# Kernel tuning notes

Hardware: AMD Instinct MI355X
Metric: run time of the kernel (lower is better)

Reference implementation:

```python
import jax, jax.numpy as jnp
import numpy as np

RES = 14
N = RES * RES
NH = 8
KD = 32
D = 128   # attn_ratio * key_dim
DH = 1024 # D * NH
DIM = 384
B = 128
SCALE = KD ** -0.5


def _bias_idxs():
    pts = [(i, j) for i in range(RES) for j in range(RES)]
    offs, idxs = {}, []
    for p1 in pts:
        for p2 in pts:
            o = (abs(p1[0] - p2[0]), abs(p1[1] - p2[1]))
            offs.setdefault(o, len(offs))
            idxs.append(offs[o])
    return np.array(idxs, np.int32).reshape(N, N), len(offs)

BIAS_IDXS, NUM_OFF = _bias_idxs()  # (N, N), 196 distinct |offset| pairs


def setup_inputs() -> dict:
    key = jax.random.key(0)
    ks = jax.random.split(key, 32)
    g = lambda i, shape, s=0.05: jax.random.normal(ks[i], shape, jnp.float32) * s
    pos = lambda i, shape: jax.random.uniform(ks[i], shape, jnp.float32, minval=0.5, maxval=1.5)
    return dict(
        x=jax.random.normal(ks[0], (B, DIM, RES, RES), jnp.float32),
        qw=g(1, (NH * KD, DIM)), qb=g(2, (NH * KD,)), q_s=pos(3, (NH * KD,)), q_t=g(4, (NH * KD,)),
        kw=g(5, (NH * KD, DIM)), kb=g(6, (NH * KD,)), k_s=pos(7, (NH * KD,)), k_t=g(8, (NH * KD,)),
        vw=g(9, (DH, DIM)), vb=g(10, (DH,)), v_s=pos(11, (DH,)), v_t=g(12, (DH,)),
        lvw=g(13, (DH, 3, 3)), lvb=g(14, (DH,)), lv_s=pos(15, (DH,)), lv_t=g(16, (DH,)),
        th1w=g(17, (NH, NH), 0.3), th1b=g(18, (NH,)),
        th2w=g(19, (NH, NH), 0.3), th2b=g(20, (NH,)),
        ab=g(21, (NH, NUM_OFF)),
        pw=g(22, (DIM, DH)), pb=g(23, (DIM,)), p_s=pos(24, (DIM,)), p_t=g(25, (DIM,)),
    )


def _c(v):
    return v[None, :, None, None]


def conv1x1_bn(x, w, b, s, t):
    # 1x1 conv (NCHW) + eval-mode BN folded to per-channel affine
    y = jnp.einsum('bchw,oc->bohw', x, w) + _c(b)
    return y * _c(s) + _c(t)


def reference(x, qw, qb, q_s, q_t, kw, kb, k_s, k_t, vw, vb, v_s, v_t,
              lvw, lvb, lv_s, lv_t, th1w, th1b, th2w, th2b, ab,
              pw, pb, p_s, p_t):
    Bb = x.shape[0]
    # q,k: (B, NH, N, KD)
    q = conv1x1_bn(x, qw, qb, q_s, q_t).reshape(Bb, NH, KD, N).transpose(0, 1, 3, 2)
    k = conv1x1_bn(x, kw, kb, k_s, k_t).reshape(Bb, NH, KD, N).transpose(0, 1, 3, 2)
    v4 = conv1x1_bn(x, vw, vb, v_s, v_t)  # (B, DH, RES, RES)
    # local depthwise 3x3 conv + BN on v
    vl = jax.lax.conv_general_dilated(
        v4, lvw.reshape(DH, 1, 3, 3), window_strides=(1, 1), padding='SAME',
        dimension_numbers=('NCHW', 'OIHW', 'NCHW'), feature_group_count=DH)
    vl = (vl + _c(lvb)) * _c(lv_s) + _c(lv_t)
    v = v4.reshape(Bb, NH, D, N).transpose(0, 1, 3, 2)  # (B, NH, N, D)

    attn = jnp.einsum('bhid,bhjd->bhij', q, k) * SCALE
    attn = attn + ab[:, BIAS_IDXS][None]  # relative-position bias (1, NH, N, N)
    attn = jnp.einsum('bhij,gh->bgij', attn, th1w) + _c(th1b)  # talking head 1
    attn = jax.nn.softmax(attn, axis=-1)
    attn = jnp.einsum('bhij,gh->bgij', attn, th2w) + _c(th2b)  # talking head 2

    o = jnp.einsum('bhij,bhjd->bhid', attn, v)  # (B, NH, N, D)
    o = o.transpose(0, 1, 3, 2).reshape(Bb, DH, RES, RES) + vl
    o = jax.nn.relu(o)
    return conv1x1_bn(o, pw, pb, p_s, p_t)
```

## Files before the change

### kernel.cpp

```cpp
#include <hip/hip_runtime.h>
#include <hip/hip_bf16.h>
#include <stdint.h>

typedef __hip_bfloat16 bf16;
typedef short short4v __attribute__((ext_vector_type(4)));
typedef short short8 __attribute__((ext_vector_type(8)));
typedef float f32x4 __attribute__((ext_vector_type(4)));

#define NB 128
#define NPIX 196
#define NPAD 208
#define VP 224
#define QROWS 208
#define NH 8
#define KD 32
#define DHEAD 128
#define DH 1024
#define DIM 384
#define SCALE 0.17677669529663687f

__device__ __forceinline__ float b2f(bf16 v) { return __bfloat162float(v); }
__device__ __forceinline__ bf16 f2b(float f) { return __float2bfloat16(f); }
__device__ __forceinline__ float us2f(unsigned short u) {
  union { unsigned int i; float f; } v; v.i = (unsigned int)u << 16; return v.f;
}
__device__ __forceinline__ short f2us(float f) {
  bf16 b = __float2bfloat16(f);
  return *(short*)&b;
}

__device__ __forceinline__ void gll16(const void* g, void* l) {
  auto gp = reinterpret_cast<const uint32_t __attribute__((address_space(1)))*>(
      reinterpret_cast<uintptr_t>(g));
  auto lp = reinterpret_cast<uint32_t __attribute__((address_space(3)))*>(
      reinterpret_cast<uintptr_t>(l));
  __builtin_amdgcn_global_load_lds(gp, lp, 16, 0, 0);
}

__global__ __launch_bounds__(256) void k_cvt4(const float* __restrict__ s0,
                                              const float* __restrict__ s1,
                                              const float* __restrict__ s2,
                                              const float* __restrict__ s3,
                                              bf16* __restrict__ dst) {
  int i = blockIdx.x * 256 + threadIdx.x;
  if (i >= 983040) return;
  const float* src; int o;
  if (i < 98304)       { src = s0; o = i; }
  else if (i < 196608) { src = s1; o = i - 98304; }
  else if (i < 589824) { src = s2; o = i - 196608; }
  else                 { src = s3; o = i - 589824; }
  dst[i] = f2b(src[o]);
}

__global__ __launch_bounds__(256) void k_xt(const float* __restrict__ x,
                                            bf16* __restrict__ XT) {
  __shared__ bf16 tile[32][33];
  int ct = blockIdx.x, nt = blockIdx.y, b = blockIdx.z;
  int c0 = ct * 32, n0 = nt * 32;
  int tc = threadIdx.x >> 5, tn = threadIdx.x & 31;
#pragma unroll
  for (int r = 0; r < 4; ++r) {
    int c = tc + r * 8;
    int n = n0 + tn;
    float v = 0.f;
    if (n < NPIX) v = x[((size_t)b * DIM + c0 + c) * NPIX + n];
    tile[c][tn] = f2b(v);
  }
  __syncthreads();
#pragma unroll
  for (int r = 0; r < 4; ++r) {
    int n = n0 + tc + r * 8;
    if (n < NPAD) XT[((size_t)b * NPAD + n) * DIM + c0 + tn] = tile[tn][tc + r * 8];
  }
}

__global__ __launch_bounds__(256, 2) void k_qkv2(
    const bf16* __restrict__ Wf, const bf16* __restrict__ XT,
    const float* __restrict__ qb, const float* __restrict__ qs, const float* __restrict__ qt,
    const float* __restrict__ kb, const float* __restrict__ ks, const float* __restrict__ kt,
    const float* __restrict__ vb, const float* __restrict__ vs, const float* __restrict__ vt,
    bf16* __restrict__ qf, bf16* __restrict__ kf, bf16* __restrict__ v4) {
  __shared__ __align__(16) char lds[2][32768];
  const int NWG = 12 * 208;
  int id = blockIdx.x;
  int id2 = (id & 7) * (NWG >> 3) + (id >> 3);
  int mt = id2 % 12, nt = id2 / 12;
  int m0 = mt * 128, n0 = nt * 128;
  int tid = threadIdx.x, lane = tid & 63;
  int wv = tid >> 6, wm = wv >> 1, wn = wv & 1;

  f32x4 acc[4][4];
#pragma unroll
  for (int mi = 0; mi < 4; ++mi)
#pragma unroll
    for (int ni = 0; ni < 4; ++ni)
#pragma unroll
      for (int r = 0; r < 4; ++r) acc[mi][ni][r] = 0.f;

  auto stage = [&](int buf, int t) {
    int k0 = t * 64;
#pragma unroll
    for (int j = 0; j < 4; ++j) {
      int gi = tid + j * 256;
      int row = gi >> 3, g = gi & 7;
      int sk = k0 + ((g ^ (row & 7)) << 3);
      gll16(Wf + (size_t)(m0 + row) * DIM + sk, &lds[buf][gi * 16]);
      gll16(XT + (size_t)(n0 + row) * DIM + sk, &lds[buf][16384 + gi * 16]);
    }
  };
  auto compute = [&](int buf) {
    const char* Ab = lds[buf];
    const char* Bb = lds[buf] + 16384;
    int kq = lane >> 4, il = lane & 15;
#pragma unroll
    for (int ksb = 0; ksb < 2; ++ksb) {
      int G = ksb * 4 + kq;
      short8 af[4], bfr[4];
#pragma unroll
      for (int mi = 0; mi < 4; ++mi) {
        int row = wm * 64 + mi * 16 + il;
        af[mi] = *(const short8*)(Ab + row * 128 + ((G ^ (row & 7)) << 4));
      }
#pragma unroll
      for (int ni = 0; ni < 4; ++ni) {
        int row = wn * 64 + ni * 16 + il;
        bfr[ni] = *(const short8*)(Bb + row * 128 + ((G ^ (row & 7)) << 4));
      }
#pragma unroll
      for (int mi = 0; mi < 4; ++mi)
#pragma unroll
        for (int ni = 0; ni < 4; ++ni)
          acc[mi][ni] = __builtin_amdgcn_mfma_f32_16x16x32_bf16(af[mi], bfr[ni], acc[mi][ni], 0, 0, 0);
    }
  };

  stage(0, 0);
  __syncthreads();
  for (int t = 0; t < 6; ++t) {
    if (t < 5) stage((t + 1) & 1, t + 1);
    compute(t & 1);
    __syncthreads();
  }

  int cq = lane >> 4, cn = lane & 15;
#pragma unroll
  for (int mi = 0; mi < 4; ++mi) {
    int mbase = m0 + wm * 64 + mi * 16;
    const float *bp, *sp, *tp;
    int segbase, segid;
    if (mbase < 256)      { bp = qb; sp = qs; tp = qt; segbase = 0;   segid = 0; }
    else if (mbase < 512) { bp = kb; sp = ks; tp = kt; segbase = 256; segid = 1; }
    else                  { bp = vb; sp = vs; tp = vt; segbase = 512; segid = 2; }
#pragma unroll
    for (int r = 0; r < 4; ++r) {
      int ms = mbase - segbase + cq * 4 + r;
      float bi = bp[ms], sc = sp[ms], tt = tp[ms];
#pragma unroll
      for (int ni = 0; ni < 4; ++ni) {
        int n = n0 + wn * 64 + ni * 16 + cn;
        int b = n / NPAD;
        int nn = n - b * NPAD;
        float y = (acc[mi][ni][r] + bi) * sc + tt;
        y = (nn < NPIX) ? y : 0.f;
        if (segid == 2) {
          v4[((size_t)b * DH + ms) * VP + nn] = f2b(y);
        } else {
          bf16* dst = segid ? kf : qf;
          dst[(((size_t)b * NH + (ms >> 5)) * QROWS + nn) * KD + (ms & 31)] = f2b(y);
        }
      }
    }
  }
}

__global__ __launch_bounds__(256) void k_vpad(bf16* __restrict__ v4) {
  int i = blockIdx.x * 256 + threadIdx.x;
  int tot = NB * DH * 16;
  if (i < tot) {
    int row = i >> 4, c = i & 15;
    v4[(size_t)row * VP + 208 + c] = f2b(0.f);
  }
}

__global__ __launch_bounds__(256, 2) void k_p2(
    const bf16* __restrict__ Pw, const bf16* __restrict__ OT,
    const float* __restrict__ pb, const float* __restrict__ ps, const float* __restrict__ pt,
    float* __restrict__ out) {
  __shared__ __align__(16) char lds[2][32768];
  const int NWG = 3 * 208;
  int id = blockIdx.x;
  int id2 = (id & 7) * (NWG >> 3) + (id >> 3);
  int mt = id2 % 3, nt = id2 / 3;
  int m0 = mt * 128, n0 = nt * 128;
  int tid = threadIdx.x, lane = tid & 63;
  int wv = tid >> 6, wm = wv >> 1, wn = wv & 1;

  f32x4 acc[4][4];
#pragma unroll
  for (int mi = 0; mi < 4; ++mi)
#pragma unroll
    for (int ni = 0; ni < 4; ++ni)
#pragma unroll
      for (int r = 0; r < 4; ++r) acc[mi][ni][r] = 0.f;

  auto stage = [&](int buf, int t) {
    int k0 = t * 64;
#pragma unroll
    for (int j = 0; j < 4; ++j) {
      int gi = tid + j * 256;
      int row = gi >> 3, g = gi & 7;
      int sk = k0 + ((g ^ (row & 7)) << 3);
      gll16(Pw + (size_t)(m0 + row) * DH + sk, &lds[buf][gi * 16]);
      gll16(OT + (size_t)(n0 + row) * DH + sk, &lds[buf][16384 + gi * 16]);
    }
  };
  auto compute = [&](int buf) {
    const char* Ab = lds[buf];
    const char* Bb = lds[buf] + 16384;
    int kq = lane >> 4, il = lane & 15;
#pragma unroll
    for (int ksb = 0; ksb < 2; ++ksb) {
      int G = ksb * 4 + kq;
      short8 af[4], bfr[4];
#pragma unroll
      for (int mi = 0; mi < 4; ++mi) {
        int row = wm * 64 + mi * 16 + il;
        af[mi] = *(const short8*)(Ab + row * 128 + ((G ^ (row & 7)) << 4));
      }
#pragma unroll
      for (int ni = 0; ni < 4; ++ni) {
        int row = wn * 64 + ni * 16 + il;
        bfr[ni] = *(const short8*)(Bb + row * 128 + ((G ^ (row & 7)) << 4));
      }
#pragma unroll
      for (int mi = 0; mi < 4; ++mi)
#pragma unroll
        for (int ni = 0; ni < 4; ++ni)
          acc[mi][ni] = __builtin_amdgcn_mfma_f32_16x16x32_bf16(af[mi], bfr[ni], acc[mi][ni], 0, 0, 0);
    }
  };

  stage(0, 0);
  __syncthreads();
  for (int t = 0; t < 16; ++t) {
    if (t < 15) stage((t + 1) & 1, t + 1);
    compute(t & 1);
    __syncthreads();
  }

  int cq = lane >> 4, cn = lane & 15;
#pragma unroll
  for (int mi = 0; mi < 4; ++mi) {
#pragma unroll
    for (int r = 0; r < 4; ++r) {
      int m = m0 + wm * 64 + mi * 16 + cq * 4 + r;
      float bi = pb[m], sc = ps[m], tt = pt[m];
#pragma unroll
      for (int ni = 0; ni < 4; ++ni) {
        int n = n0 + wn * 64 + ni * 16 + cn;
        int b = n / NPAD;
        int nn = n - b * NPAD;
        if (nn < NPIX)
          out[((size_t)b * DIM + m) * NPIX + nn] = (acc[mi][ni][r] + bi) * sc + tt;
      }
    }
  }
}

__global__ __launch_bounds__(256) void k_dwv(
    const bf16* __restrict__ v4, const float* __restrict__ lvw,
    const float* __restrict__ lvb, const float* __restrict__ lvs,
    const float* __restrict__ lvt, bf16* __restrict__ vl,
    float* __restrict__ vcs) {
  int blk = blockIdx.x;
  int b = blk >> 8, cg = blk & 255;
  int lc = threadIdx.x >> 6, px = threadIdx.x & 63;
  int ch = cg * 4 + lc;
  const bf16* src = v4 + ((size_t)b * DH + ch) * VP;
  float w[9];
#pragma unroll
  for (int i = 0; i < 9; ++i) w[i] = lvw[ch * 9 + i];
  float bb = lvb[ch], ss = lvs[ch], tt = lvt[ch];
  bf16* dst = vl + ((size_t)b * DH + ch) * NPIX;
  float csum = 0.f;
  for (int p = px; p < NPIX; p += 64) {
    int ri = p / 14, ci = p - ri * 14;
    float s = 0.f;
#pragma unroll
    for (int dy = -1; dy <= 1; ++dy)
#pragma unroll
      for (int dx = -1; dx <= 1; ++dx) {
        int rr = ri + dy, cc = ci + dx;
        if (rr >= 0 && rr < 14 && cc >= 0 && cc < 14)
          s += w[(dy + 1) * 3 + dx + 1] * b2f(src[rr * 14 + cc]);
      }
    csum += b2f(src[p]);
    dst[p] = f2b((s + bb) * ss + tt);
  }
  csum += __shfl_xor(csum, 1);
  csum += __shfl_xor(csum, 2);
  csum += __shfl_xor(csum, 4);
  csum += __shfl_xor(csum, 8);
  csum += __shfl_xor(csum, 16);
  csum += __shfl_xor(csum, 32);
  if (px == 0) vcs[b * DH + ch] = csum;
}

#define SROW 448
__device__ __forceinline__ int saddr(int g, int i, int j) {
  int r = j * 2 + ((i & 7) << 4);
  if (r >= SROW) r -= SROW;
  return (g * 16 + i) * SROW + r;
}

__global__ __launch_bounds__(512, 2) void k_att(
    const bf16* __restrict__ qf, const bf16* __restrict__ kf,
    const bf16* __restrict__ v4, const bf16* __restrict__ vl,
    const float* __restrict__ vcs,
    const float* __restrict__ th1w, const float* __restrict__ th1b,
    const float* __restrict__ th2w, const float* __restrict__ th2b,
    const float* __restrict__ ab, bf16* __restrict__ OT) {
  __shared__ __align__(16) char smem[NH * 16 * SROW];
  __shared__ float ab2[NH * NPIX];
  __shared__ float c1s[64];
  __shared__ float c2s[64];
  __shared__ float smInv[NH * 16];
  int id = blockIdx.x;
  int xcd = id & 7;
  int rest = id >> 3;
  int qt = rest % 13;
  int b = (rest / 13) * 8 + xcd;
  int i0 = qt * 16;
  int tid = threadIdx.x;
  int wave = tid >> 6, lane = tid & 63;
  int il = lane & 15, kh = lane >> 4;

  if (tid < 64) {
    c1s[tid] = th1w[tid] * SCALE;
    c2s[tid] = th2w[tid];
  }
  for (int pos = tid; pos < NH * NPIX; pos += 512) {
    int g = pos / NPIX, off = pos - g * NPIX;
    float s = th1b[g];
#pragma unroll
    for (int h = 0; h < 8; ++h)
      s += th1w[g * 8 + h] * ab[h * NPIX + off];
    ab2[pos] = s;
  }
  {
    const bf16* qp = qf + ((size_t)b * NH + wave) * QROWS * KD;
    const bf16* kp = kf + ((size_t)b * NH + wave) * QROWS * KD;
    short8 a = *(const short8*)(qp + (i0 + il) * KD + kh * 8);
    for (int jt = 0; jt < 13; ++jt) {
      short8 bb = *(const short8*)(kp + (jt * 16 + il) * KD + kh * 8);
      f32x4 acc = {0.f, 0.f, 0.f, 0.f};
      acc = __builtin_amdgcn_mfma_f32_16x16x32_bf16(a, bb, acc, 0, 0, 0);
      int j = jt * 16 + il;
#pragma unroll
      for (int r = 0; r < 4; ++r)
        *(bf16*)(smem + saddr(wave, kh * 4 + r, j)) = f2b(acc[r]);
    }
  }
  __syncthreads();
  for (int pos = tid; pos < 16 * NPIX; pos += 512) {
    int i = pos / NPIX, j = pos - i * NPIX;
    float sv[8];
#pragma unroll
    for (int h = 0; h < 8; ++h) sv[h] = b2f(*(const bf16*)(smem + saddr(h, i, j)));
    int ia = i0 + i; if (ia > 195) ia = 195;
    int ri = ia / 14, ci = ia - ri * 14;
    int rj = j / 14, cj = j - rj * 14;
    int dr = ri > rj ? ri - rj : rj - ri;
    int dc = ci > cj ? ci - cj : cj - ci;
    int off = dr * 14 + dc;
    float outv[8];
#pragma unroll
    for (int g = 0; g < 8; ++g) {
      float s = ab2[g * NPIX + off];
#pragma unroll
      for (int h = 0; h < 8; ++h) s += c1s[g * 8 + h] * sv[h];
      outv[g] = s;
    }
#pragma unroll
    for (int g = 0; g < 8; ++g)
      *(bf16*)(smem + saddr(g, i, j)) = f2b(outv[g]);
  }
  __syncthreads();
  {
    int row = tid >> 2, part = tid & 3;
    int g = row >> 4, i = row & 15;
    int jb = part * 52;
    int n4 = (part == 3) ? 10 : 13;
    float m = -1e30f;
    for (int it = 0; it < n4; ++it) {
      short4v v = *(const short4v*)(smem + saddr(g, i, jb + it * 4));
#pragma unroll
      for (int t = 0; t < 4; ++t) m = fmaxf(m, us2f((unsigned short)v[t]));
    }
    m = fmaxf(m, __shfl_xor(m, 1));
    m = fmaxf(m, __shfl_xor(m, 2));
    float s = 0.f;
    for (int it = 0; it < n4; ++it) {
      char* p = smem + saddr(g, i, jb + it * 4);
      short4v v = *(const short4v*)p;
      short4v w;
#pragma unroll
      for (int t = 0; t < 4; ++t) {
        float e = __expf(us2f((unsigned short)v[t]) - m);
        s += e;
        w[t] = f2us(e);
      }
      *(short4v*)p = w;
    }
    if (part == 3) {
      short4v z = {0, 0, 0, 0};
#pragma unroll
      for (int it = 0; it < 7; ++it)
        *(short4v*)(smem + saddr(g, i, 196 + it * 4)) = z;
    }
    s += __shfl_xor(s, 1);
    s += __shfl_xor(s, 2);
    if (part == 0) smInv[row] = 1.f / s;
  }
  __syncthreads();
  for (int pos = tid; pos < 16 * NPIX; pos += 512) {
    int i = pos / NPIX, j = pos - i * NPIX;
    float pv[8];
#pragma unroll
    for (int g = 0; g < 8; ++g)
      pv[g] = b2f(*(const bf16*)(smem + saddr(g, i, j))) * smInv[g * 16 + i];
#pragma unroll
    for (int g2 = 0; g2 < 8; ++g2) {
      float s = 0.f;
#pragma unroll
      for (int g = 0; g < 8; ++g) s += c2s[g2 * 8 + g] * pv[g];
      *(bf16*)(smem + saddr(g2, i, j)) = f2b(s);
    }
  }
  __syncthreads();
  {
    int g = wave;
    f32x4 oacc[8];
#pragma unroll
    for (int dt = 0; dt < 8; ++dt)
#pragma unroll
      for (int r = 0; r < 4; ++r) oacc[dt][r] = 0.f;
    const bf16* vbase = v4 + ((size_t)b * DH + g * DHEAD) * VP;
    for (int ks = 0; ks < 7; ++ks) {
      short8 pa = *(const short8*)(smem + saddr(g, il, ks * 32 + kh * 8));
#pragma unroll
      for (int dt = 0; dt < 8; ++dt) {
        short8 bv = *(const short8*)(vbase + (size_t)(dt * 16 + il) * VP + ks * 32 + kh * 8);
        oacc[dt] = __builtin_amdgcn_mfma_f32_16x16x32_bf16(pa, bv, oacc[dt], 0, 0, 0);
      }
    }
    float t2b = th2b[g];
#pragma unroll
    for (int dt = 0; dt < 8; ++dt) {
      int ch = g * DHEAD + dt * 16 + il;
      float csv = vcs[b * DH + ch] * t2b;
#pragma unroll
      for (int r = 0; r < 4; ++r) {
        int n = i0 + kh * 4 + r;
        if (n < NPIX) {
          float val = oacc[dt][r] + csv + b2f(vl[((size_t)b * DH + ch) * NPIX + n]);
          OT[((size_t)b * NPAD + n) * DH + ch] = f2b(fmaxf(val, 0.f));
        } else {
          OT[((size_t)b * NPAD + n) * DH + ch] = f2b(0.f);
        }
      }
    }
  }
}

extern "C" void kernel_launch(void* const* d_in, const int* in_sizes, int n_in,
                              void* d_out, int out_size, void* d_ws, size_t ws_size,
                              hipStream_t stream) {
  const float* x    = (const float*)d_in[0];
  const float* qw   = (const float*)d_in[1];
  const float* qb   = (const float*)d_in[2];
  const float* q_s  = (const float*)d_in[3];
  const float* q_t  = (const float*)d_in[4];
  const float* kw   = (const float*)d_in[5];
  const float* kb   = (const float*)d_in[6];
  const float* k_s  = (const float*)d_in[7];
  const float* k_t  = (const float*)d_in[8];
  const float* vw   = (const float*)d_in[9];
  const float* vb   = (const float*)d_in[10];
  const float* v_s  = (const float*)d_in[11];
  const float* v_t  = (const float*)d_in[12];
  const float* lvw  = (const float*)d_in[13];
  const float* lvb  = (const float*)d_in[14];
  const float* lv_s = (const float*)d_in[15];
  const float* lv_t = (const float*)d_in[16];
  const float* th1w = (const float*)d_in[17];
  const float* th1b = (const float*)d_in[18];
  const float* th2w = (const float*)d_in[19];
  const float* th2b = (const float*)d_in[20];
  const float* ab   = (const float*)d_in[21];
  const float* pw   = (const float*)d_in[22];
  const float* pb   = (const float*)d_in[23];
  const float* p_s  = (const float*)d_in[24];
  const float* p_t  = (const float*)d_in[25];

  char* ws = (char*)d_ws;
  size_t off = 0;
  auto alloc = [&](size_t bytes) {
    char* p = ws + off;
    off += (bytes + 255) & ~(size_t)255;
    return p;
  };
  char* region0 = alloc((size_t)NB * NPAD * DH * 2);
  bf16* XT  = (bf16*)region0;
  bf16* OT  = (bf16*)region0;
  bf16* qfb = (bf16*)alloc((size_t)NB * NH * QROWS * KD * 2);
  bf16* kfb = (bf16*)alloc((size_t)NB * NH * QROWS * KD * 2);
  bf16* v4  = (bf16*)alloc((size_t)NB * DH * VP * 2);
  bf16* vlb = (bf16*)alloc((size_t)NB * DH * NPIX * 2);
  float* vcs = (float*)alloc((size_t)NB * DH * 4);
  bf16* wf  = (bf16*)alloc((size_t)1536 * DIM * 2);
  bf16* wpb = (bf16*)alloc((size_t)DIM * DH * 2);
  (void)ws_size; (void)in_sizes; (void)n_in; (void)out_size;

  k_cvt4<<<dim3(3840), 256, 0, stream>>>(qw, kw, vw, pw, wf);
  k_xt<<<dim3(12, 7, NB), 256, 0, stream>>>(x, XT);
  k_qkv2<<<dim3(2496), 256, 0, stream>>>(wf, XT, qb, q_s, q_t, kb, k_s, k_t,
                                         vb, v_s, v_t, qfb, kfb, v4);
  k_vpad<<<dim3((NB * DH * 16 + 255) / 256), 256, 0, stream>>>(v4);
  k_dwv<<<dim3(NB * 256), 256, 0, stream>>>(v4, lvw, lvb, lv_s, lv_t, vlb, vcs);
  k_att<<<dim3(1664), 512, 0, stream>>>(qfb, kfb, v4, vlb, vcs,
                                        th1w, th1b, th2w, th2b, ab, OT);
  k_p2<<<dim3(624), 256, 0, stream>>>(wpb, OT, pb, p_s, p_t, (float*)d_out);
}
```

Baseline: 437.1 us.

## Precompute bias tables once, shrink attention LDS, use 32x32 MFMA for PV

The per-block talking-head bias table and scaled weights are now computed once in an extra block of the weight-conversion kernel, so the attention kernel no longer spends its prologue rebuilding them and no longer holds them in LDS. The V row pad is reduced from 224 to 208, which removes the k_vpad kernel, and the LDS score row is shrunk so more blocks can share a CU (launch bounds raised to 6). The PV product is reorganised around 32x32x16 MFMAs with V as the A operand over 13 k-steps. In exchange, half the lanes sit idle in the epilogue, weights are read from global or constant memory instead of LDS, and register pressure under the higher occupancy target may cause spills.

```diff
diff --git a/kernel.cpp b/kernel.cpp
--- a/kernel.cpp
+++ b/kernel.cpp
@@ -6,11 +6,12 @@
 typedef short short4v __attribute__((ext_vector_type(4)));
 typedef short short8 __attribute__((ext_vector_type(8)));
 typedef float f32x4 __attribute__((ext_vector_type(4)));
+typedef float f32x16 __attribute__((ext_vector_type(16)));
 
 #define NB 128
 #define NPIX 196
 #define NPAD 208
-#define VP 224
+#define VP 208
 #define QROWS 208
 #define NH 8
 #define KD 32
@@ -41,9 +42,26 @@
                                               const float* __restrict__ s1,
                                               const float* __restrict__ s2,
                                               const float* __restrict__ s3,
-                                              bf16* __restrict__ dst) {
+                                              bf16* __restrict__ dst,
+                                              const float* __restrict__ th1w,
+                                              const float* __restrict__ th1b,
+                                              const float* __restrict__ ab,
+                                              float* __restrict__ ab2g,
+                                              float* __restrict__ c1g) {
+  if (blockIdx.x >= 3840) {
+    int t = threadIdx.x;
+    for (int pos = t; pos < NH * NPIX; pos += 256) {
+      int g = pos / NPIX, off = pos - g * NPIX;
+      float s = th1b[g];
+#pragma unroll
+      for (int h = 0; h < 8; ++h)
+        s += th1w[g * 8 + h] * ab[h * NPIX + off];
+      ab2g[pos] = s;
+    }
+    if (t < 64) c1g[t] = th1w[t] * SCALE;
+    return;
+  }
   int i = blockIdx.x * 256 + threadIdx.x;
-  if (i >= 983040) return;
   const float* src; int o;
   if (i < 98304)       { src = s0; o = i; }
   else if (i < 196608) { src = s1; o = i - 98304; }
@@ -173,15 +191,6 @@
   }
 }
 
-__global__ __launch_bounds__(256) void k_vpad(bf16* __restrict__ v4) {
-  int i = blockIdx.x * 256 + threadIdx.x;
-  int tot = NB * DH * 16;
-  if (i < tot) {
-    int row = i >> 4, c = i & 15;
-    v4[(size_t)row * VP + 208 + c] = f2b(0.f);
-  }
-}
-
 __global__ __launch_bounds__(256, 2) void k_p2(
     const bf16* __restrict__ Pw, const bf16* __restrict__ OT,
     const float* __restrict__ pb, const float* __restrict__ ps, const float* __restrict__ pt,
@@ -306,24 +315,21 @@
   if (px == 0) vcs[b * DH + ch] = csum;
 }
 
-#define SROW 448
+#define SROW 416
 __device__ __forceinline__ int saddr(int g, int i, int j) {
   int r = j * 2 + ((i & 7) << 4);
   if (r >= SROW) r -= SROW;
   return (g * 16 + i) * SROW + r;
 }
 
-__global__ __launch_bounds__(512, 2) void k_att(
+__global__ __launch_bounds__(512, 6) void k_att(
     const bf16* __restrict__ qf, const bf16* __restrict__ kf,
     const bf16* __restrict__ v4, const bf16* __restrict__ vl,
     const float* __restrict__ vcs,
-    const float* __restrict__ th1w, const float* __restrict__ th1b,
+    const float* __restrict__ ab2g, const float* __restrict__ c1g,
     const float* __restrict__ th2w, const float* __restrict__ th2b,
-    const float* __restrict__ ab, bf16* __restrict__ OT) {
+    bf16* __restrict__ OT) {
   __shared__ __align__(16) char smem[NH * 16 * SROW];
-  __shared__ float ab2[NH * NPIX];
-  __shared__ float c1s[64];
-  __shared__ float c2s[64];
   __shared__ float smInv[NH * 16];
   int id = blockIdx.x;
   int xcd = id & 7;
@@ -335,18 +341,6 @@
   int wave = tid >> 6, lane = tid & 63;
   int il = lane & 15, kh = lane >> 4;
 
-  if (tid < 64) {
-    c1s[tid] = th1w[tid] * SCALE;
-    c2s[tid] = th2w[tid];
-  }
-  for (int pos = tid; pos < NH * NPIX; pos += 512) {
-    int g = pos / NPIX, off = pos - g * NPIX;
-    float s = th1b[g];
-#pragma unroll
-    for (int h = 0; h < 8; ++h)
-      s += th1w[g * 8 + h] * ab[h * NPIX + off];
-    ab2[pos] = s;
-  }
   {
     const bf16* qp = qf + ((size_t)b * NH + wave) * QROWS * KD;
     const bf16* kp = kf + ((size_t)b * NH + wave) * QROWS * KD;
@@ -376,9 +370,9 @@
     float outv[8];
 #pragma unroll
     for (int g = 0; g < 8; ++g) {
-      float s = ab2[g * NPIX + off];
-#pragma unroll
-      for (int h = 0; h < 8; ++h) s += c1s[g * 8 + h] * sv[h];
+      float s = ab2g[g * NPIX + off];
+#pragma unroll
+      for (int h = 0; h < 8; ++h) s += c1g[g * 8 + h] * sv[h];
       outv[g] = s;
     }
 #pragma unroll
@@ -415,7 +409,7 @@
     if (part == 3) {
       short4v z = {0, 0, 0, 0};
 #pragma unroll
-      for (int it = 0; it < 7; ++it)
+      for (int it = 0; it < 3; ++it)
         *(short4v*)(smem + saddr(g, i, 196 + it * 4)) = z;
     }
     s += __shfl_xor(s, 1);
@@ -433,40 +427,42 @@
     for (int g2 = 0; g2 < 8; ++g2) {
       float s = 0.f;
 #pragma unroll
-      for (int g = 0; g < 8; ++g) s += c2s[g2 * 8 + g] * pv[g];
+      for (int g = 0; g < 8; ++g) s += th2w[g2 * 8 + g] * pv[g];
       *(bf16*)(smem + saddr(g2, i, j)) = f2b(s);
     }
   }
   __syncthreads();
   {
     int g = wave;
-    f32x4 oacc[8];
-#pragma unroll
-    for (int dt = 0; dt < 8; ++dt)
-#pragma unroll
-      for (int r = 0; r < 4; ++r) oacc[dt][r] = 0.f;
-    const bf16* vbase = v4 + ((size_t)b * DH + g * DHEAD) * VP;
-    for (int ks = 0; ks < 7; ++ks) {
-      short8 pa = *(const short8*)(smem + saddr(g, il, ks * 32 + kh * 8));
-#pragma unroll
-      for (int dt = 0; dt < 8; ++dt) {
-        short8 bv = *(const short8*)(vbase + (size_t)(dt * 16 + il) * VP + ks * 32 + kh * 8);
-        oacc[dt] = __builtin_amdgcn_mfma_f32_16x16x32_bf16(pa, bv, oacc[dt], 0, 0, 0);
-      }
-    }
+    int cl = lane & 31, s = lane >> 5;
+    const bf16* vb0 = v4 + ((size_t)b * DH + g * DHEAD) * VP;
     float t2b = th2b[g];
 #pragma unroll
-    for (int dt = 0; dt < 8; ++dt) {
-      int ch = g * DHEAD + dt * 16 + il;
-      float csv = vcs[b * DH + ch] * t2b;
-#pragma unroll
-      for (int r = 0; r < 4; ++r) {
-        int n = i0 + kh * 4 + r;
-        if (n < NPIX) {
-          float val = oacc[dt][r] + csv + b2f(vl[((size_t)b * DH + ch) * NPIX + n]);
-          OT[((size_t)b * NPAD + n) * DH + ch] = f2b(fmaxf(val, 0.f));
-        } else {
-          OT[((size_t)b * NPAD + n) * DH + ch] = f2b(0.f);
+    for (int dt2 = 0; dt2 < 4; ++dt2) {
+      f32x16 acc;
+#pragma unroll
+      for (int r = 0; r < 16; ++r) acc[r] = 0.f;
+      const bf16* vrow = vb0 + (size_t)(dt2 * 32 + cl) * VP + s * 8;
+      const char* prow = smem + (size_t)0;
+      for (int ks = 0; ks < 13; ++ks) {
+        short8 av = *(const short8*)(vrow + ks * 16);
+        short8 bp = *(const short8*)(smem + saddr(g, cl & 15, ks * 16 + s * 8));
+        acc = __builtin_amdgcn_mfma_f32_32x32x16_bf16(av, bp, acc, 0, 0, 0);
+      }
+      (void)prow;
+      if (cl < 16) {
+        int n = i0 + cl;
+#pragma unroll
+        for (int reg = 0; reg < 16; ++reg) {
+          int chs = dt2 * 32 + (reg & 3) + 8 * (reg >> 2) + 4 * s;
+          int ch = g * DHEAD + chs;
+          if (n < NPIX) {
+            float val = acc[reg] + vcs[b * DH + ch] * t2b +
+                        b2f(vl[((size_t)b * DH + ch) * NPIX + n]);
+            OT[((size_t)b * NPAD + n) * DH + ch] = f2b(fmaxf(val, 0.f));
+          } else {
+            OT[((size_t)b * NPAD + n) * DH + ch] = f2b(0.f);
+          }
         }
       }
     }
@@ -520,15 +516,17 @@
   float* vcs = (float*)alloc((size_t)NB * DH * 4);
   bf16* wf  = (bf16*)alloc((size_t)1536 * DIM * 2);
   bf16* wpb = (bf16*)alloc((size_t)DIM * DH * 2);
+  float* ab2g = (float*)alloc((size_t)NH * NPIX * 4);
+  float* c1g  = (float*)alloc((size_t)64 * 4);
   (void)ws_size; (void)in_sizes; (void)n_in; (void)out_size;
 
-  k_cvt4<<<dim3(3840), 256, 0, stream>>>(qw, kw, vw, pw, wf);
+  k_cvt4<<<dim3(3841), 256, 0, stream>>>(qw, kw, vw, pw, wf, th1w, th1b, ab,
+                                         ab2g, c1g);
   k_xt<<<dim3(12, 7, NB), 256, 0, stream>>>(x, XT);
   k_qkv2<<<dim3(2496), 256, 0, stream>>>(wf, XT, qb, q_s, q_t, kb, k_s, k_t,
                                          vb, v_s, v_t, qfb, kfb, v4);
-  k_vpad<<<dim3((NB * DH * 16 + 255) / 256), 256, 0, stream>>>(v4);
   k_dwv<<<dim3(NB * 256), 256, 0, stream>>>(v4, lvw, lvb, lv_s, lv_t, vlb, vcs);
   k_att<<<dim3(1664), 512, 0, stream>>>(qfb, kfb, v4, vlb, vcs,
-                                        th1w, th1b, th2w, th2b, ab, OT);
+                                        ab2g, c1g, th2w, th2b, OT);
   k_p2<<<dim3(624), 256, 0, stream>>>(wpb, OT, pb, p_s, p_t, (float*)d_out);
 }
```

After: 495.7 us. 1.13x slower.
